# Kernel tuning notes

Hardware: AMD Instinct MI355X
Metric: run time of the kernel (lower is better)

## Reference

```python
import jax, jax.numpy as jnp
import numpy as np

HID = 1024
BATCH = 32
SRC = 2048

def setup_inputs() -> dict:
    key = jax.random.key(0)
    k1, k2, k3, k4, k5 = jax.random.split(key, 5)
    hidden = jax.random.normal(k1, (BATCH, HID), dtype=jnp.float32)
    encoder_outputs = jax.random.normal(k2, (BATCH, SRC, HID), dtype=jnp.float32)
    # nn.Linear(2H, H): weight [H, 2H], bias [H]
    lim = 1.0 / np.sqrt(2 * HID)
    attn_w = jax.random.uniform(k3, (HID, 2 * HID), dtype=jnp.float32, minval=-lim, maxval=lim)
    attn_b = jax.random.uniform(k4, (HID,), dtype=jnp.float32, minval=-lim, maxval=lim)
    v = jax.random.uniform(k5, (HID,), dtype=jnp.float32)  # torch.rand
    return {"hidden": hidden, "encoder_outputs": encoder_outputs,
            "attn_w": attn_w, "attn_b": attn_b, "v": v}

def reference(hidden, encoder_outputs, attn_w, attn_b, v):
    # Split the concat linear: cat([hidden, enc]) @ W^T == hidden @ Wh^T + enc @ We^T
    w_h = attn_w[:, :HID]          # [H, H] acts on repeated hidden
    w_e = attn_w[:, HID:]          # [H, H] acts on encoder outputs
    # energy: [B, S, H]
    energy = jnp.tanh(
        jnp.einsum('bh,oh->bo', hidden, w_h)[:, None, :]
        + jnp.einsum('bsh,oh->bso', encoder_outputs, w_e)
        + attn_b
    )
    scores = jnp.einsum('bso,o->bs', energy, v)  # [B, S]
    return jax.nn.softmax(scores, axis=1)
```

## Files before the change

### kernel.cpp

```cpp
#include <hip/hip_runtime.h>
#include <hip/hip_bf16.h>

#define HID    1024
#define NBATCH 32
#define SRC    2048
#define MROWS  (NBATCH * SRC)

typedef _Float16 f16;
typedef f16   f16x8 __attribute__((ext_vector_type(8)));
typedef f16   f16x4 __attribute__((ext_vector_type(4)));
typedef float f32x4 __attribute__((ext_vector_type(4)));

#define BAR()    __builtin_amdgcn_s_barrier()
#define LGKM0()  asm volatile("s_waitcnt lgkmcnt(0)")
#define VMCNT0() asm volatile("s_waitcnt vmcnt(0)")
#define SCHED0() __builtin_amdgcn_sched_barrier(0)

__device__ __forceinline__ void gload_lds16(const void* g, void* l) {
  __builtin_amdgcn_global_load_lds(
      (const __attribute__((address_space(1))) void*)g,
      (__attribute__((address_space(3))) void*)l, 16, 0, 0);
}

__device__ __forceinline__ float fast_tanh(float x) {
  x = fminf(fmaxf(x, -15.f), 15.f);
  float e = __expf(2.f * x);
  return (e - 1.f) / (e + 1.f);
}

__global__ void convw_k(const float* __restrict__ attn_w, f16* __restrict__ Wf) {
  int idx = blockIdx.x * 256 + threadIdx.x;
  int j = idx * 4;
  int o = j >> 10, h = j & 1023;
  f32x4 d = *(const f32x4*)(attn_w + (size_t)o * 2048 + HID + h);
  f16x4 q = { (f16)d[0], (f16)d[1], (f16)d[2], (f16)d[3] };
  *(f16x4*)(Wf + (size_t)o * HID + h) = q;
}

__global__ void hvec_k(const float* __restrict__ hidden,
                       const float* __restrict__ attn_w,
                       const float* __restrict__ attn_b,
                       float* __restrict__ hvec) {
  int idx = blockIdx.x * 256 + threadIdx.x;
  int b = idx >> 10, o = idx & 1023;
  const float* wrow = attn_w + (size_t)o * 2048;
  const float* hrow = hidden + (size_t)b * HID;
  float acc = 0.f;
  for (int h = 0; h < HID; h += 4) {
    f32x4 wv = *(const f32x4*)(wrow + h);
    f32x4 hv = *(const f32x4*)(hrow + h);
    acc += wv[0]*hv[0] + wv[1]*hv[1] + wv[2]*hv[2] + wv[3]*hv[3];
  }
  hvec[idx] = acc + attn_b[o];
}

__global__ void convA_k(const float* __restrict__ A, f16* __restrict__ Af) {
  size_t i = ((size_t)blockIdx.x * 256 + threadIdx.x) * 8;
  f32x4 d0 = *(const f32x4*)(A + i);
  f32x4 d1 = *(const f32x4*)(A + i + 4);
  f16x8 q = { (f16)d0[0], (f16)d0[1], (f16)d0[2], (f16)d0[3],
              (f16)d1[0], (f16)d1[1], (f16)d1[2], (f16)d1[3] };
  *(f16x8*)(Af + i) = q;
}


#define STG_A(Tn, cd) do { \
  _Pragma("unroll") for (int q_ = 0; q_ < 4; ++q_) \
    gload_lds16(Ab + (size_t)(q_ * 64 + (tid >> 3)) * HID + (Tn) * 64 + scol, \
                lds + (cd) * 65536 + q_ * 8192 + w * 1024); } while (0)
#define STG_B(Tn, cd) do { \
  _Pragma("unroll") for (int q_ = 0; q_ < 4; ++q_) \
    gload_lds16(Bb + (size_t)(q_ * 64 + (tid >> 3)) * HID + (Tn) * 64 + scol, \
                lds + (cd) * 65536 + 32768 + q_ * 8192 + w * 1024); } while (0)

#define RD_A(la_, mh_) do { \
  _Pragma("unroll") for (int m4 = 0; m4 < 4; ++m4) { \
    const char* rb = (la_) + (wr * 128 + (mh_) * 64 + m4 * 16 + lr) * 128; \
    aF[m4][0] = *(const f16x8*)(rb + ((lg ^ sw) << 4)); \
    aF[m4][1] = *(const f16x8*)(rb + (((4 + lg) ^ sw) << 4)); } } while (0)
#define RD_B(lb_, dst, nh_) do { \
  _Pragma("unroll") for (int n2 = 0; n2 < 2; ++n2) { \
    const char* rb = (lb_) + (wc * 64 + (nh_) * 32 + n2 * 16 + lr) * 128; \
    dst[n2][0] = *(const f16x8*)(rb + ((lg ^ sw) << 4)); \
    dst[n2][1] = *(const f16x8*)(rb + (((4 + lg) ^ sw) << 4)); } } while (0)

#define MFMA16(bsrc, mo, no) do { \
  __builtin_amdgcn_s_setprio(1); \
  _Pragma("unroll") for (int ks = 0; ks < 2; ++ks) \
  _Pragma("unroll") for (int m4 = 0; m4 < 4; ++m4) \
  _Pragma("unroll") for (int n2 = 0; n2 < 2; ++n2) \
    acc[(mo) + m4][(no) + n2] = __builtin_amdgcn_mfma_f32_16x16x32_f16( \
        aF[m4][ks], bsrc[n2][ks], acc[(mo) + m4][(no) + n2], 0, 0, 0); \
  __builtin_amdgcn_s_setprio(0); } while (0)

#define TILE(c, Tn, DOSTG) do { \
  const char* la_ = lds + (c) * 65536; \
  const char* lb_ = la_ + 32768; \
   \
  RD_A(la_, 0); RD_B(lb_, bF0, 0); \
  if (DOSTG) STG_A(Tn, (c) ^ 1); \
  BAR(); LGKM0(); SCHED0(); \
  MFMA16(bF0, 0, 0); \
  BAR(); SCHED0(); \
   \
  RD_B(lb_, bF1, 1); \
  if (DOSTG) STG_B(Tn, (c) ^ 1); \
  BAR(); LGKM0(); SCHED0(); \
  MFMA16(bF1, 0, 2); \
  BAR(); SCHED0(); \
   \
  RD_A(la_, 1); \
  BAR(); LGKM0(); SCHED0(); \
  MFMA16(bF1, 4, 2); \
  BAR(); SCHED0(); \
   \
  MFMA16(bF0, 4, 0); \
  if (DOSTG) { VMCNT0(); SCHED0(); } \
  BAR(); SCHED0(); \
} while (0)

__global__ __launch_bounds__(512, 2) void gemm_f16(
    const f16*  __restrict__ Af,
    const f16*  __restrict__ Wf,
    const float* __restrict__ hvec,
    const float* __restrict__ v,
    float* __restrict__ part)
{
  extern __shared__ __align__(16) char lds[];

  int bid = blockIdx.x;
  int wg = (bid & 7) * 128 + (bid >> 3);
  int m_idx = wg >> 2, n_idx = wg & 3;
  long row0 = (long)m_idx * 256;
  int o0 = n_idx * 256;
  int b = (int)(row0 >> 11);

  int tid = threadIdx.x;
  int l = tid & 63, w = tid >> 6;
  int wr = w >> 2, wc = w & 3;
  int lr = l & 15, lg = l >> 4;
  int sw = lr & 7;
  int scol = ((tid & 7) ^ ((tid >> 3) & 7)) * 8;

  const f16* Ab = Af + row0 * HID;
  const f16* Bb = Wf + (size_t)o0 * HID;

  f32x4 acc[8][4];
#pragma unroll
  for (int m = 0; m < 8; ++m)
#pragma unroll
    for (int n = 0; n < 4; ++n) acc[m][n] = (f32x4){0.f, 0.f, 0.f, 0.f};

  f16x8 aF[4][2], bF0[2][2], bF1[2][2];

  STG_A(0, 0); STG_B(0, 0);
  VMCNT0(); SCHED0(); BAR(); SCHED0();

#pragma unroll 1
  for (int Tp = 0; Tp < 8; ++Tp) {
    const int Ta = Tp * 2, Tb = Ta + 1;
    TILE(0, Ta + 1, 1);
    TILE(1, Tb + 1, (Tb < 15));
  }

  float hvv[4], vvv[4];
#pragma unroll
  for (int n = 0; n < 4; ++n) {
    int o = o0 + wc * 64 + n * 16 + lr;
    hvv[n] = hvec[b * HID + o];
    vvv[n] = v[o];
  }
  float* scf = (float*)lds;
  __syncthreads();
#pragma unroll
  for (int m = 0; m < 8; ++m) {
#pragma unroll
    for (int r = 0; r < 4; ++r) {
      float s = 0.f;
#pragma unroll
      for (int n = 0; n < 4; ++n)
        s += fast_tanh(acc[m][n][r] + hvv[n]) * vvv[n];
      s += __shfl_xor(s, 1); s += __shfl_xor(s, 2);
      s += __shfl_xor(s, 4); s += __shfl_xor(s, 8);
      if (lr == 0) scf[wc * 256 + wr * 128 + m * 16 + lg * 4 + r] = s;
    }
  }
  __syncthreads();
  if (tid < 256)
    part[(size_t)n_idx * MROWS + row0 + tid] =
        scf[tid] + scf[256 + tid] + scf[512 + tid] + scf[768 + tid];
}

__global__ __launch_bounds__(256, 2) void gemm_fb(
    const float* __restrict__ A, const f16* __restrict__ Wf,
    const float* __restrict__ hvec, const float* __restrict__ v,
    float* __restrict__ part)
{
  __shared__ __align__(16) f16 lA[128][32];
  __shared__ __align__(16) f16 lB[128][32];
  __shared__ float sc[128];

  int bid = blockIdx.x;
  int x = bid & 7, j = bid >> 3;
  int m_idx = x * 64 + (j >> 3);
  int n_idx = j & 7;
  long row0 = (long)m_idx * 128;
  int o0 = n_idx * 128;
  int b = (int)(row0 >> 11);

  int tid = threadIdx.x;
  int l = tid & 63, w = tid >> 6;
  int wr = w >> 1, wc = w & 1;
  int lr = l & 15, lg = l >> 4;

  f32x4 acc[4][4];
#pragma unroll
  for (int m = 0; m < 4; ++m)
#pragma unroll
    for (int n = 0; n < 4; ++n) acc[m][n] = (f32x4){0.f, 0.f, 0.f, 0.f};

  const float* Abase = A + row0 * 1024;

  for (int k0 = 0; k0 < 1024; k0 += 32) {
    __syncthreads();
#pragma unroll
    for (int i = 0; i < 2; ++i) {
      int rr = (i * 256 + tid) >> 2;
      const f16* src = Wf + (size_t)(o0 + rr) * HID + k0 + (tid & 3) * 8;
      char* ldsb = (char*)&lB[0][0] + i * 4096 + w * 1024;
      gload_lds16(src, ldsb);
    }
#pragma unroll
    for (int i = 0; i < 4; ++i) {
      int ja = i * 256 + tid;
      int arow = ja >> 3, ac4 = ja & 7;
      f32x4 d = *(const f32x4*)(Abase + (size_t)arow * 1024 + k0 + ac4 * 4);
      f16x4 q = { (f16)d[0], (f16)d[1], (f16)d[2], (f16)d[3] };
      *(f16x4*)&lA[arow][ac4 * 4] = q;
    }
    __syncthreads();
    f16x8 aF[4], bF[4];
#pragma unroll
    for (int m = 0; m < 4; ++m)
      aF[m] = *(const f16x8*)&lA[wr * 64 + m * 16 + lr][lg * 8];
#pragma unroll
    for (int n = 0; n < 4; ++n)
      bF[n] = *(const f16x8*)&lB[wc * 64 + n * 16 + lr][lg * 8];
#pragma unroll
    for (int m = 0; m < 4; ++m)
#pragma unroll
      for (int n = 0; n < 4; ++n)
        acc[m][n] = __builtin_amdgcn_mfma_f32_16x16x32_f16(aF[m], bF[n], acc[m][n], 0, 0, 0);
  }

  float hv[4], vv[4];
#pragma unroll
  for (int n = 0; n < 4; ++n) {
    int o = o0 + wc * 64 + n * 16 + lr;
    hv[n] = hvec[b * HID + o];
    vv[n] = v[o];
  }
  float myv[4][4];
#pragma unroll
  for (int m = 0; m < 4; ++m) {
#pragma unroll
    for (int r = 0; r < 4; ++r) {
      float s = 0.f;
#pragma unroll
      for (int n = 0; n < 4; ++n)
        s += fast_tanh(acc[m][n][r] + hv[n]) * vv[n];
      s += __shfl_xor(s, 1); s += __shfl_xor(s, 2);
      s += __shfl_xor(s, 4); s += __shfl_xor(s, 8);
      myv[m][r] = s;
    }
  }
  if (wc == 0 && lr == 0) {
#pragma unroll
    for (int m = 0; m < 4; ++m)
#pragma unroll
      for (int r = 0; r < 4; ++r)
        sc[wr * 64 + m * 16 + lg * 4 + r] = myv[m][r];
  }
  __syncthreads();
  if (wc == 1 && lr == 0) {
#pragma unroll
    for (int m = 0; m < 4; ++m)
#pragma unroll
      for (int r = 0; r < 4; ++r)
        sc[wr * 64 + m * 16 + lg * 4 + r] += myv[m][r];
  }
  __syncthreads();
  if (tid < 128)
    part[(size_t)n_idx * MROWS + row0 + tid] = sc[tid];
}

__global__ void softmax_k(const float* __restrict__ part, float* __restrict__ out,
                          int nsl) {
  int b = blockIdx.x;
  __shared__ float srow[SRC];
  __shared__ float red[8];
  int tid = threadIdx.x;

  float lmax = -1e30f;
  for (int i = tid; i < SRC; i += 256) {
    float s = 0.f;
    for (int t = 0; t < nsl; ++t)
      s += part[(size_t)t * MROWS + (size_t)b * SRC + i];
    srow[i] = s;
    lmax = fmaxf(lmax, s);
  }
#pragma unroll
  for (int off = 32; off >= 1; off >>= 1)
    lmax = fmaxf(lmax, __shfl_xor(lmax, off));
  if ((tid & 63) == 0) red[tid >> 6] = lmax;
  __syncthreads();
  float bmax = fmaxf(fmaxf(red[0], red[1]), fmaxf(red[2], red[3]));

  float lsum = 0.f;
  for (int i = tid; i < SRC; i += 256) {
    float e = __expf(srow[i] - bmax);
    srow[i] = e;
    lsum += e;
  }
#pragma unroll
  for (int off = 32; off >= 1; off >>= 1)
    lsum += __shfl_xor(lsum, off);
  if ((tid & 63) == 0) red[4 + (tid >> 6)] = lsum;
  __syncthreads();
  float inv = 1.f / (red[4] + red[5] + red[6] + red[7]);
  for (int i = tid; i < SRC; i += 256)
    out[(size_t)b * SRC + i] = srow[i] * inv;
}

extern "C" void kernel_launch(void* const* d_in, const int* in_sizes, int n_in,
                              void* d_out, int out_size, void* d_ws, size_t ws_size,
                              hipStream_t stream) {
  const float* hidden = (const float*)d_in[0];
  const float* enc    = (const float*)d_in[1];
  const float* attn_w = (const float*)d_in[2];
  const float* attn_b = (const float*)d_in[3];
  const float* v      = (const float*)d_in[4];
  float* out = (float*)d_out;

  char* ws = (char*)d_ws;
  f16*   Wf   = (f16*)ws;
  float* hv   = (float*)(ws + (2ull << 20));
  float* part = (float*)(ws + (2ull << 20) + (128ull << 10));
  f16*   Af   = (f16*)(ws + (8ull << 20));

  const size_t WS_NEEDED = (8ull << 20) + (128ull << 20);

  convw_k<<<1024, 256, 0, stream>>>(attn_w, Wf);
  hvec_k <<<128,  256, 0, stream>>>(hidden, attn_w, attn_b, hv);

  if (ws_size >= WS_NEEDED) {
    convA_k<<<32768, 256, 0, stream>>>(enc, Af);
    gemm_f16<<<1024, 512, 131072, stream>>>(Af, Wf, hv, v, part);
    softmax_k<<<NBATCH, 256, 0, stream>>>(part, out, 4);
  } else {
    gemm_fb<<<4096, 256, 0, stream>>>(enc, Wf, hv, v, part);
    softmax_k<<<NBATCH, 256, 0, stream>>>(part, out, 8);
  }
}
```

Before: 291.7 us.

## Spread global-to-LDS staging across MFMA phases with partial vmcnt waits

Splits each tile's A and B global-to-LDS loads into eight per-unit issues and interleaves them two at a time across the four MFMA phases of the loop. The first units of the following tile are issued early, and the full vmcnt(0) drain is replaced by vmcnt(2), so prefetch loads stay in flight across tile boundaries. This aims to smooth memory issue and hide load latency behind compute. The cost is tighter correctness reasoning about the double-buffer hazard, because loads into one LDS buffer are issued while the other buffer's loads are still outstanding.

```diff
diff --git a/kernel.cpp b/kernel.cpp
--- a/kernel.cpp
+++ b/kernel.cpp
@@ -13,8 +13,8 @@
 
 #define BAR()    __builtin_amdgcn_s_barrier()
 #define LGKM0()  asm volatile("s_waitcnt lgkmcnt(0)")
-#define VMCNT0() asm volatile("s_waitcnt vmcnt(0)")
 #define SCHED0() __builtin_amdgcn_sched_barrier(0)
+#define VMC(n)   asm volatile("s_waitcnt vmcnt(" #n ")")
 
 __device__ __forceinline__ void gload_lds16(const void* g, void* l) {
   __builtin_amdgcn_global_load_lds(
@@ -64,60 +64,32 @@
 }
 
 
-#define STG_A(Tn, cd) do { \
-  _Pragma("unroll") for (int q_ = 0; q_ < 4; ++q_) \
-    gload_lds16(Ab + (size_t)(q_ * 64 + (tid >> 3)) * HID + (Tn) * 64 + scol, \
-                lds + (cd) * 65536 + q_ * 8192 + w * 1024); } while (0)
-#define STG_B(Tn, cd) do { \
-  _Pragma("unroll") for (int q_ = 0; q_ < 4; ++q_) \
-    gload_lds16(Bb + (size_t)(q_ * 64 + (tid >> 3)) * HID + (Tn) * 64 + scol, \
-                lds + (cd) * 65536 + 32768 + q_ * 8192 + w * 1024); } while (0)
+#define STG1(u, Tn) do { \
+  const f16* s_ = ((u) < 4 ? Ab : Bb) + \
+      (size_t)(((u) & 3) * 64 + (tid >> 3)) * HID + (Tn) * 64 + scol; \
+  char* d_ = lds + ((Tn) & 1) * 65536 + ((u) < 4 ? 0 : 32768) + ((u) & 3) * 8192 + w * 1024; \
+  gload_lds16(s_, d_); } while (0)
 
 #define RD_A(la_, mh_) do { \
   _Pragma("unroll") for (int m4 = 0; m4 < 4; ++m4) { \
     const char* rb = (la_) + (wr * 128 + (mh_) * 64 + m4 * 16 + lr) * 128; \
     aF[m4][0] = *(const f16x8*)(rb + ((lg ^ sw) << 4)); \
     aF[m4][1] = *(const f16x8*)(rb + (((4 + lg) ^ sw) << 4)); } } while (0)
+
 #define RD_B(lb_, dst, nh_) do { \
   _Pragma("unroll") for (int n2 = 0; n2 < 2; ++n2) { \
     const char* rb = (lb_) + (wc * 64 + (nh_) * 32 + n2 * 16 + lr) * 128; \
     dst[n2][0] = *(const f16x8*)(rb + ((lg ^ sw) << 4)); \
     dst[n2][1] = *(const f16x8*)(rb + (((4 + lg) ^ sw) << 4)); } } while (0)
 
-#define MFMA16(bsrc, mo, no) do { \
+#define MFMA16(bsrc, mh_, nh_) do { \
   __builtin_amdgcn_s_setprio(1); \
   _Pragma("unroll") for (int ks = 0; ks < 2; ++ks) \
   _Pragma("unroll") for (int m4 = 0; m4 < 4; ++m4) \
   _Pragma("unroll") for (int n2 = 0; n2 < 2; ++n2) \
-    acc[(mo) + m4][(no) + n2] = __builtin_amdgcn_mfma_f32_16x16x32_f16( \
-        aF[m4][ks], bsrc[n2][ks], acc[(mo) + m4][(no) + n2], 0, 0, 0); \
+    acc[(mh_) * 4 + m4][(nh_) * 2 + n2] = __builtin_amdgcn_mfma_f32_16x16x32_f16( \
+        aF[m4][ks], bsrc[n2][ks], acc[(mh_) * 4 + m4][(nh_) * 2 + n2], 0, 0, 0); \
   __builtin_amdgcn_s_setprio(0); } while (0)
-
-#define TILE(c, Tn, DOSTG) do { \
-  const char* la_ = lds + (c) * 65536; \
-  const char* lb_ = la_ + 32768; \
-   \
-  RD_A(la_, 0); RD_B(lb_, bF0, 0); \
-  if (DOSTG) STG_A(Tn, (c) ^ 1); \
-  BAR(); LGKM0(); SCHED0(); \
-  MFMA16(bF0, 0, 0); \
-  BAR(); SCHED0(); \
-   \
-  RD_B(lb_, bF1, 1); \
-  if (DOSTG) STG_B(Tn, (c) ^ 1); \
-  BAR(); LGKM0(); SCHED0(); \
-  MFMA16(bF1, 0, 2); \
-  BAR(); SCHED0(); \
-   \
-  RD_A(la_, 1); \
-  BAR(); LGKM0(); SCHED0(); \
-  MFMA16(bF1, 4, 2); \
-  BAR(); SCHED0(); \
-   \
-  MFMA16(bF0, 4, 0); \
-  if (DOSTG) { VMCNT0(); SCHED0(); } \
-  BAR(); SCHED0(); \
-} while (0)
 
 __global__ __launch_bounds__(512, 2) void gemm_f16(
     const f16*  __restrict__ Af,
@@ -145,6 +117,11 @@
   const f16* Ab = Af + row0 * HID;
   const f16* Bb = Wf + (size_t)o0 * HID;
 
+  const char* la0 = lds;
+  const char* lb0 = lds + 32768;
+  const char* la1 = lds + 65536;
+  const char* lb1 = lds + 98304;
+
   f32x4 acc[8][4];
 #pragma unroll
   for (int m = 0; m < 8; ++m)
@@ -153,14 +130,54 @@
 
   f16x8 aF[4][2], bF0[2][2], bF1[2][2];
 
-  STG_A(0, 0); STG_B(0, 0);
-  VMCNT0(); SCHED0(); BAR(); SCHED0();
+  STG1(0, 0); STG1(1, 0); STG1(2, 0); STG1(3, 0);
+  STG1(4, 0); STG1(5, 0); STG1(6, 0); STG1(7, 0);
+  STG1(0, 1); STG1(1, 1);
+  VMC(2); SCHED0(); BAR();
 
 #pragma unroll 1
-  for (int Tp = 0; Tp < 8; ++Tp) {
-    const int Ta = Tp * 2, Tb = Ta + 1;
-    TILE(0, Ta + 1, 1);
-    TILE(1, Tb + 1, (Tb < 15));
+  for (int E = 0; E < 16; E += 2) {
+    const int LAST = (E == 14);
+    RD_A(la0, 0); RD_B(lb0, bF0, 0);
+    STG1(2, E + 1); STG1(3, E + 1);
+    SCHED0(); BAR(); LGKM0(); SCHED0();
+    MFMA16(bF0, 0, 0);
+    BAR();
+    RD_B(lb0, bF1, 1);
+    STG1(4, E + 1); STG1(5, E + 1);
+    SCHED0(); BAR(); LGKM0(); SCHED0();
+    MFMA16(bF1, 0, 1);
+    BAR();
+    RD_A(la0, 1);
+    STG1(6, E + 1); STG1(7, E + 1);
+    SCHED0(); BAR(); LGKM0(); SCHED0();
+    MFMA16(bF1, 1, 1);
+    BAR();
+    if (!LAST) { STG1(0, E + 2); STG1(1, E + 2); }
+    SCHED0(); BAR(); LGKM0(); SCHED0();
+    MFMA16(bF0, 1, 0);
+    if (!LAST) { VMC(2); } else { VMC(0); }
+    SCHED0(); BAR();
+    RD_A(la1, 0); RD_B(lb1, bF0, 0);
+    if (!LAST) { STG1(2, E + 2); STG1(3, E + 2); }
+    SCHED0(); BAR(); LGKM0(); SCHED0();
+    MFMA16(bF0, 0, 0);
+    BAR();
+    RD_B(lb1, bF1, 1);
+    if (!LAST) { STG1(4, E + 2); STG1(5, E + 2); }
+    SCHED0(); BAR(); LGKM0(); SCHED0();
+    MFMA16(bF1, 0, 1);
+    BAR();
+    RD_A(la1, 1);
+    if (!LAST) { STG1(6, E + 2); STG1(7, E + 2); }
+    SCHED0(); BAR(); LGKM0(); SCHED0();
+    MFMA16(bF1, 1, 1);
+    BAR();
+    if (!LAST) { STG1(0, E + 3); STG1(1, E + 3); }
+    SCHED0(); BAR(); LGKM0(); SCHED0();
+    MFMA16(bF0, 1, 0);
+    if (!LAST) { VMC(2); SCHED0(); }
+    BAR();
   }
 
   float hvv[4], vvv[4];
```

Measured after the change: 286.5 us. About the same (-1.8%).
